# Performance work log

Measured on AMD Instinct MI355X. Metric: run time of the kernel, lower is better.

The kernel has to match this reference:

```python
import jax, jax.numpy as jnp
import numpy as np

HEADS = 4
DIM_HEAD = 64
EPS = 1e-12  # F.normalize clamp_min eps

def _l2norm(t):
    n = jnp.sqrt(jnp.sum(t * t, axis=-1, keepdims=True))
    return t / jnp.maximum(n, EPS)

def _dwconv3d(x, w, groups):
    # x: [b, c, d, h, w]; w: [c, 1, 3, 3, 3]
    return jax.lax.conv_general_dilated(
        x, w, window_strides=(1, 1, 1),
        padding=((1, 1), (1, 1), (1, 1)),
        dimension_numbers=('NCDHW', 'OIDHW', 'NCDHW'),
        feature_group_count=groups)

def setup_inputs() -> dict:
    key = jax.random.key(0)
    ks = jax.random.split(key, 6)
    dim, inner = 64, HEADS * DIM_HEAD
    x_in = jax.random.normal(ks[0], (1, 8, 128, 128, dim), jnp.float32)
    w_qkv = jax.random.normal(ks[1], (dim, 3 * inner), jnp.float32) * 0.05
    rescale = jnp.ones((HEADS, 1, 1), jnp.float32)
    w_proj = jax.random.normal(ks[2], (inner, dim), jnp.float32) * 0.05
    b_proj = jax.random.normal(ks[3], (dim,), jnp.float32) * 0.01
    w_pe1 = jax.random.normal(ks[4], (dim, 1, 3, 3, 3), jnp.float32) * 0.1
    w_pe2 = jax.random.normal(ks[5], (dim, 1, 3, 3, 3), jnp.float32) * 0.1
    return {"x_in": x_in, "w_qkv": w_qkv, "rescale": rescale,
            "w_proj": w_proj, "b_proj": b_proj, "w_pe1": w_pe1, "w_pe2": w_pe2}

def reference(x_in, w_qkv, rescale, w_proj, b_proj, w_pe1, w_pe2):
    b, d, h, w, c = x_in.shape
    N = d * h * w
    inner = HEADS * DIM_HEAD
    x = x_in.reshape(b, N, c)
    qkv = x @ w_qkv  # [b, N, 3*inner]
    q, k, v = jnp.split(qkv, 3, axis=-1)
    # [b, N, inner] -> [b, heads, dim_head, N]
    to_hdn = lambda t: t.reshape(b, N, HEADS, DIM_HEAD).transpose(0, 2, 3, 1)
    q, k, v = to_hdn(q), to_hdn(k), to_hdn(v)
    q = _l2norm(q)
    k = _l2norm(k)
    attn = jnp.einsum('bhdn,bhen->bhde', k, q)  # [b, heads, dd, dd]
    attn = attn * rescale[None]
    attn = jax.nn.softmax(attn, axis=-1)
    xo = jnp.einsum('bhde,bhen->bhdn', attn, v)  # [b, heads, dd, N]
    xo = xo.transpose(0, 3, 1, 2).reshape(b, N, inner)  # (h dd) channel order
    out_c = (xo @ w_proj + b_proj).reshape(b, d, h, w, c)
    # positional branch: depthwise conv3d -> GELU -> depthwise conv3d
    xp = x_in.transpose(0, 4, 1, 2, 3)  # [b, c, d, h, w]
    xp = _dwconv3d(xp, w_pe1, c)
    xp = jax.nn.gelu(xp, approximate=False)
    xp = _dwconv3d(xp, w_pe2, c)
    out_p = xp.transpose(0, 2, 3, 4, 1)
    return out_c + out_p
```

## Files before the change

kernel.cpp:

```cpp
#include <hip/hip_runtime.h>
#include <hip/hip_bf16.h>
#include <math.h>


#define NTOK 131072

typedef __attribute__((ext_vector_type(8))) short short8v;
typedef __attribute__((ext_vector_type(4))) float f32x4;

__device__ __forceinline__ uint32_t pk2(float a, float b) {
    return ((__float_as_uint(a) + 0x8000u) >> 16) |
           (((__float_as_uint(b) + 0x8000u) >> 16) << 16);
}
__device__ __forceinline__ float bl(uint32_t w) { return __uint_as_float(w << 16); }
__device__ __forceinline__ float bh(uint32_t w) { return __uint_as_float(w & 0xFFFF0000u); }

__global__ __launch_bounds__(256) void k_gram(const float* __restrict__ x,
                                              float* __restrict__ partial) {
    const int tid = threadIdx.x;
    const int lane = tid & 63;
    const int wave = tid >> 6;
    const int gwave = blockIdx.x * 4 + wave;
    const int lh = lane >> 4;
    const int lc = lane & 15;
    f32x4 acc[10];
#pragma unroll
    for (int t = 0; t < 10; ++t) acc[t] = (f32x4){0.f, 0.f, 0.f, 0.f};
    const long tokBase = (long)gwave * 64;
#pragma unroll
    for (int s = 0; s < 2; ++s) {
        const long t0 = tokBase + s * 32 + lh * 8;
        float v[4][8];
#pragma unroll
        for (int r = 0; r < 4; ++r) {
            const float* p = x + t0 * 64 + r * 16 + lc;
#pragma unroll
            for (int i = 0; i < 8; ++i) v[r][i] = p[i * 64];
        }
        union { short8v s8; uint32_t u[4]; } fh[4], fl[4];
#pragma unroll
        for (int r = 0; r < 4; ++r) {
#pragma unroll
            for (int w = 0; w < 4; ++w) {
                const float a = v[r][2 * w], b = v[r][2 * w + 1];
                const uint32_t hw = pk2(a, b);
                fh[r].u[w] = hw;
                fl[r].u[w] = pk2(a - bl(hw), b - bh(hw));
            }
        }
#pragma unroll
        for (int td = 0; td < 4; ++td) {
#pragma unroll
            for (int te = td; te < 4; ++te) {
                const int t = td * 4 + te - (td * (td + 1)) / 2;
                acc[t] = __builtin_amdgcn_mfma_f32_16x16x32_bf16(fh[td].s8, fh[te].s8, acc[t], 0, 0, 0);
                acc[t] = __builtin_amdgcn_mfma_f32_16x16x32_bf16(fh[td].s8, fl[te].s8, acc[t], 0, 0, 0);
                acc[t] = __builtin_amdgcn_mfma_f32_16x16x32_bf16(fl[td].s8, fh[te].s8, acc[t], 0, 0, 0);
            }
        }
    }
    float* pb = partial + (size_t)gwave * 2560;
#pragma unroll
    for (int t = 0; t < 10; ++t)
#pragma unroll
        for (int j = 0; j < 4; ++j)
            pb[t * 256 + (lh * 4 + j) * 16 + lc] = acc[t][j];
}

__global__ __launch_bounds__(256) void k_reduceG(const float* __restrict__ partial,
                                                 float* __restrict__ G) {
    const int entry = (blockIdx.x & 15) * 256 + threadIdx.x;
    const int slice = blockIdx.x >> 4;
    const int d = entry >> 6, e = entry & 63;
    int td = d >> 4, te = e >> 4, r = d & 15, c = e & 15;
    if (td > te) { int t = td; td = te; te = t; t = r; r = c; c = t; }
    const int off = (td * 4 + te - (td * (td + 1)) / 2) * 256 + r * 16 + c;
    const float* p = partial + (size_t)slice * 64 * 2560 + off;
    float s = 0.f;
#pragma unroll 8
    for (int i = 0; i < 64; ++i) s += p[(size_t)i * 2560];
    atomicAdd(&G[entry], s);
}

__global__ __launch_bounds__(512) void k_attn(const float* __restrict__ G,
                                              const float* __restrict__ w_qkv,
                                              const float* __restrict__ rescale,
                                              const float* __restrict__ w_proj,
                                              float* __restrict__ wf) {
    __shared__ float smem[6 * 4096 + 64 * 65];
    float (*Gs)[64] = (float(*)[64])smem;
    float (*PT)[64] = (float(*)[64])smem;
    float (*Bq)[64] = (float(*)[64])(smem + 4096);
    float (*Bk)[64] = (float(*)[64])(smem + 8192);
    float (*Bp)[64] = (float(*)[64])(smem + 12288);
    float (*M1)[64] = (float(*)[64])(smem + 16384);
    float (*M2)[64] = (float(*)[64])(smem + 20480);
    float (*Sb)[65] = (float(*)[65])(smem + 24576);
    __shared__ float qin[64], kin[64];

    const int h = blockIdx.x;
    const int tid = threadIdx.x;
    const int lane = tid & 63;
    const int g = tid >> 6;
    const int p0 = g * 8;

    for (int idx = tid; idx < 4096; idx += 512) {
        const int a = idx >> 6, e = idx & 63;
        Gs[a][e] = G[idx];
        Bq[a][e] = w_qkv[a * 768 + h * 64 + e];
        Bk[a][e] = w_qkv[a * 768 + 256 + h * 64 + e];
        Bp[a][e] = w_proj[(h * 64 + a) * 64 + e];
    }
    __syncthreads();

    {
        float acc[8];
#pragma unroll
        for (int i = 0; i < 8; ++i) acc[i] = 0.f;
        for (int a = 0; a < 64; ++a) {
            const float r = Bq[a][lane];
            const float4 l0 = *(const float4*)&Gs[a][p0];
            const float4 l1 = *(const float4*)&Gs[a][p0 + 4];
            acc[0] += l0.x * r; acc[1] += l0.y * r; acc[2] += l0.z * r; acc[3] += l0.w * r;
            acc[4] += l1.x * r; acc[5] += l1.y * r; acc[6] += l1.z * r; acc[7] += l1.w * r;
        }
#pragma unroll
        for (int i = 0; i < 8; ++i) M1[p0 + i][lane] = acc[i];
    }
    {
        float acc[8];
#pragma unroll
        for (int i = 0; i < 8; ++i) acc[i] = 0.f;
        for (int a = 0; a < 64; ++a) {
            const float r = Bk[a][lane];
            const float4 l0 = *(const float4*)&Gs[a][p0];
            const float4 l1 = *(const float4*)&Gs[a][p0 + 4];
            acc[0] += l0.x * r; acc[1] += l0.y * r; acc[2] += l0.z * r; acc[3] += l0.w * r;
            acc[4] += l1.x * r; acc[5] += l1.y * r; acc[6] += l1.z * r; acc[7] += l1.w * r;
        }
#pragma unroll
        for (int i = 0; i < 8; ++i) M2[p0 + i][lane] = acc[i];
    }
    __syncthreads();

    if (tid < 64) {
        float s = 0.f;
        for (int a = 0; a < 64; ++a) s += Bq[a][tid] * M1[a][tid];
        qin[tid] = 1.f / fmaxf(sqrtf(s), 1e-12f);
    } else if (tid < 128) {
        const int d = tid - 64;
        float s = 0.f;
        for (int a = 0; a < 64; ++a) s += Bk[a][d] * M2[a][d];
        kin[d] = 1.f / fmaxf(sqrtf(s), 1e-12f);
    }
    __syncthreads();

    const float rs = rescale[h];
    {
        float acc[8];
#pragma unroll
        for (int i = 0; i < 8; ++i) acc[i] = 0.f;
        for (int a = 0; a < 64; ++a) {
            const float r = M1[a][lane];
            const float4 l0 = *(const float4*)&Bk[a][p0];
            const float4 l1 = *(const float4*)&Bk[a][p0 + 4];
            acc[0] += l0.x * r; acc[1] += l0.y * r; acc[2] += l0.z * r; acc[3] += l0.w * r;
            acc[4] += l1.x * r; acc[5] += l1.y * r; acc[6] += l1.z * r; acc[7] += l1.w * r;
        }
        const float qv = qin[lane] * rs;
#pragma unroll
        for (int i = 0; i < 8; ++i) Sb[p0 + i][lane] = acc[i] * (kin[p0 + i] * qv);
    }
    for (int idx = tid; idx < 4096; idx += 512) {
        const int a = idx >> 6, e = idx & 63;
        Bq[e][a] = w_qkv[a * 768 + 512 + h * 64 + e];
    }
    __syncthreads();

    if (tid < 64) {
        const int d = tid;
        float m = -1e30f;
        for (int e = 0; e < 64; ++e) m = fmaxf(m, Sb[d][e]);
        float s = 0.f;
        for (int e = 0; e < 64; ++e) {
            const float pv = expf(Sb[d][e] - m);
            s += pv;
            PT[e][d] = pv;
        }
        const float inv = 1.f / s;
        for (int e = 0; e < 64; ++e) PT[e][d] *= inv;
    }
    __syncthreads();

    {
        float acc[8];
#pragma unroll
        for (int i = 0; i < 8; ++i) acc[i] = 0.f;
        for (int e = 0; e < 64; ++e) {
            const float r = Bq[e][lane];
            const float4 l0 = *(const float4*)&PT[e][p0];
            const float4 l1 = *(const float4*)&PT[e][p0 + 4];
            acc[0] += l0.x * r; acc[1] += l0.y * r; acc[2] += l0.z * r; acc[3] += l0.w * r;
            acc[4] += l1.x * r; acc[5] += l1.y * r; acc[6] += l1.z * r; acc[7] += l1.w * r;
        }
        __syncthreads();
#pragma unroll
        for (int i = 0; i < 8; ++i) M2[p0 + i][lane] = acc[i];
    }
    __syncthreads();

    {
        float acc[8];
#pragma unroll
        for (int i = 0; i < 8; ++i) acc[i] = 0.f;
        for (int d = 0; d < 64; ++d) {
            const float r = Bp[d][lane];
            const float4 l0 = *(const float4*)&M2[d][p0];
            const float4 l1 = *(const float4*)&M2[d][p0 + 4];
            acc[0] += l0.x * r; acc[1] += l0.y * r; acc[2] += l0.z * r; acc[3] += l0.w * r;
            acc[4] += l1.x * r; acc[5] += l1.y * r; acc[6] += l1.z * r; acc[7] += l1.w * r;
        }
#pragma unroll
        for (int i = 0; i < 8; ++i) atomicAdd(&wf[(p0 + i) * 64 + lane], acc[i]);
    }
}

__global__ __launch_bounds__(256) void k_out(const float* __restrict__ x,
                                             const float* __restrict__ wf_g,
                                             const float* __restrict__ b_proj,
                                             float* __restrict__ out) {
    const int tid = threadIdx.x;
    const int lane = tid & 63;
    const int wave = tid >> 6;
    const int lr = lane & 15;
    const int kg = lane >> 4;

    union { short8v s8; uint32_t u[4]; } wfh[2][4], wfl[2][4];
#pragma unroll
    for (int ks = 0; ks < 2; ++ks)
#pragma unroll
        for (int nt = 0; nt < 4; ++nt)
#pragma unroll
            for (int w = 0; w < 4; ++w) {
                const int k0 = ks * 32 + kg * 8 + 2 * w;
                const float a = wf_g[k0 * 64 + nt * 16 + lr];
                const float b = wf_g[(k0 + 1) * 64 + nt * 16 + lr];
                const uint32_t hw = pk2(a, b);
                wfh[ks][nt].u[w] = hw;
                wfl[ks][nt].u[w] = pk2(a - bl(hw), b - bh(hw));
            }
    float bb[4];
#pragma unroll
    for (int nt = 0; nt < 4; ++nt) bb[nt] = b_proj[nt * 16 + lr];

    const long strip0 = ((long)blockIdx.x * 4 + wave) * 2;
#pragma unroll
    for (int s = 0; s < 2; ++s) {
        const long tok0 = (strip0 + s) * 16;
        union { short8v s8; uint32_t u[4]; } ah[2], al[2];
#pragma unroll
        for (int ks = 0; ks < 2; ++ks) {
            const float* p = x + (tok0 + lr) * 64 + ks * 32 + kg * 8;
            const float4 a0 = *(const float4*)p;
            const float4 a1 = *(const float4*)(p + 4);
            const float va[8] = {a0.x, a0.y, a0.z, a0.w, a1.x, a1.y, a1.z, a1.w};
#pragma unroll
            for (int w = 0; w < 4; ++w) {
                const uint32_t hw = pk2(va[2 * w], va[2 * w + 1]);
                ah[ks].u[w] = hw;
                al[ks].u[w] = pk2(va[2 * w] - bl(hw), va[2 * w + 1] - bh(hw));
            }
        }
        f32x4 acc[4];
#pragma unroll
        for (int nt = 0; nt < 4; ++nt) acc[nt] = (f32x4){0.f, 0.f, 0.f, 0.f};
#pragma unroll
        for (int ks = 0; ks < 2; ++ks)
#pragma unroll
            for (int nt = 0; nt < 4; ++nt) {
                acc[nt] = __builtin_amdgcn_mfma_f32_16x16x32_bf16(ah[ks].s8, wfh[ks][nt].s8, acc[nt], 0, 0, 0);
                acc[nt] = __builtin_amdgcn_mfma_f32_16x16x32_bf16(ah[ks].s8, wfl[ks][nt].s8, acc[nt], 0, 0, 0);
                acc[nt] = __builtin_amdgcn_mfma_f32_16x16x32_bf16(al[ks].s8, wfh[ks][nt].s8, acc[nt], 0, 0, 0);
            }
#pragma unroll
        for (int nt = 0; nt < 4; ++nt)
#pragma unroll
            for (int j = 0; j < 4; ++j)
                out[(tok0 + kg * 4 + j) * 64 + nt * 16 + lr] = acc[nt][j] + bb[nt];
    }
}

__global__ __launch_bounds__(256) void k_conv(const float* __restrict__ x,
                                              const float* __restrict__ w1,
                                              const float* __restrict__ w2,
                                              float* __restrict__ out) {
    __shared__ float xt[12][12][8][10];
    __shared__ uint32_t y1[10][10][8][5];
    const int tid = threadIdx.x;
    const int b = blockIdx.x;
    const int xcd = b & 7, seq = (b >> 3) & 31, cg = b >> 8;
    const int tile = xcd * 32 + seq;
    const int tw = tile & 15, th = tile >> 4;
    const int h0 = th * 8, w0 = tw * 8;
    const int c = tid & 7;
    const int cglob = cg * 8 + c;

    float wr1[27];
#pragma unroll
    for (int o = 0; o < 27; ++o) wr1[o] = w1[cglob * 27 + o];

    for (int e = tid; e < 1152; e += 256) {
        const int sp = e >> 3;
        const int hh = sp / 12;
        const int ww = sp - hh * 12;
        const int gh = h0 + hh - 2, gw = w0 + ww - 2;
        float col[10];
#pragma unroll
        for (int i = 0; i < 10; ++i) col[i] = 0.f;
        if ((unsigned)gh < 128u && (unsigned)gw < 128u) {
            const float* xp = x + ((long)gh * 128 + gw) * 64 + cglob;
#pragma unroll
            for (int gd = 0; gd < 8; ++gd) col[gd + 1] = xp[(long)gd * 1048576];
        }
        float* dst = &xt[hh][ww][e & 7][0];
#pragma unroll
        for (int i = 0; i < 5; ++i) *(float2*)(dst + 2 * i) = make_float2(col[2 * i], col[2 * i + 1]);
    }
    __syncthreads();

    for (int e = tid; e < 800; e += 256) {
        const int sp = e >> 3;
        const int hi_ = sp / 10;
        const int wi = sp - hi_ * 10;
        const int ghp = h0 + hi_ - 1, gwp = w0 + wi - 1;
        uint32_t ow_[5];
        if ((unsigned)ghp < 128u && (unsigned)gwp < 128u) {
            float acc[8];
#pragma unroll
            for (int j = 0; j < 8; ++j) acc[j] = 0.f;
#pragma unroll
            for (int oh = 0; oh < 3; ++oh) {
#pragma unroll
                for (int ow = 0; ow < 3; ++ow) {
                    const float* cp = &xt[hi_ + oh][wi + ow][e & 7][0];
                    float xc[10];
#pragma unroll
                    for (int s2 = 0; s2 < 5; ++s2) {
                        const float2 t = *(const float2*)(cp + 2 * s2);
                        xc[2 * s2] = t.x; xc[2 * s2 + 1] = t.y;
                    }
                    const float wg0 = wr1[oh * 3 + ow];
                    const float wg1 = wr1[9 + oh * 3 + ow];
                    const float wg2 = wr1[18 + oh * 3 + ow];
#pragma unroll
                    for (int j = 0; j < 8; ++j)
                        acc[j] += wg0 * xc[j] + wg1 * xc[j + 1] + wg2 * xc[j + 2];
                }
            }
            float gl[8];
#pragma unroll
            for (int j = 0; j < 8; ++j)
                gl[j] = 0.5f * acc[j] * (1.f + erff(acc[j] * 0.70710678118654752f));
            ow_[0] = pk2(0.f, gl[0]);
            ow_[1] = pk2(gl[1], gl[2]);
            ow_[2] = pk2(gl[3], gl[4]);
            ow_[3] = pk2(gl[5], gl[6]);
            ow_[4] = pk2(gl[7], 0.f);
        } else {
#pragma unroll
            for (int i = 0; i < 5; ++i) ow_[i] = 0u;
        }
        uint32_t* dst = &y1[hi_][wi][e & 7][0];
#pragma unroll
        for (int i = 0; i < 5; ++i) dst[i] = ow_[i];
    }

    float wr2[27];
#pragma unroll
    for (int o = 0; o < 27; ++o) wr2[o] = w2[cglob * 27 + o];
    __syncthreads();

    for (int e = tid; e < 512; e += 256) {
        const int sp = e >> 3;
        const int ho = sp >> 3, wo = sp & 7;
        float a2[8];
#pragma unroll
        for (int j = 0; j < 8; ++j) a2[j] = 0.f;
#pragma unroll
        for (int oh = 0; oh < 3; ++oh) {
#pragma unroll
            for (int ow = 0; ow < 3; ++ow) {
                const uint32_t* cp = &y1[ho + oh][wo + ow][e & 7][0];
                float yc[10];
#pragma unroll
                for (int wdx = 0; wdx < 5; ++wdx) {
                    const uint32_t wv = cp[wdx];
                    yc[2 * wdx] = bl(wv);
                    yc[2 * wdx + 1] = bh(wv);
                }
                const float wg0 = wr2[oh * 3 + ow];
                const float wg1 = wr2[9 + oh * 3 + ow];
                const float wg2 = wr2[18 + oh * 3 + ow];
#pragma unroll
                for (int j = 0; j < 8; ++j)
                    a2[j] += wg0 * yc[j] + wg1 * yc[j + 1] + wg2 * yc[j + 2];
            }
        }
        const int gh = h0 + ho, gw = w0 + wo;
        float* op = out + ((long)gh * 128 + gw) * 64 + cglob;
#pragma unroll
        for (int j = 0; j < 8; ++j) op[(long)j * 1048576] += a2[j];
    }
}

extern "C" void kernel_launch(void* const* d_in, const int* in_sizes, int n_in,
                              void* d_out, int out_size, void* d_ws, size_t ws_size,
                              hipStream_t stream) {
    const float* x       = (const float*)d_in[0];
    const float* w_qkv   = (const float*)d_in[1];
    const float* rescale = (const float*)d_in[2];
    const float* w_proj  = (const float*)d_in[3];
    const float* b_proj  = (const float*)d_in[4];
    const float* w_pe1   = (const float*)d_in[5];
    const float* w_pe2   = (const float*)d_in[6];
    float* out = (float*)d_out;

    float* G  = (float*)d_ws;
    float* wf = G + 4096;
    float* partial = out;

    hipMemsetAsync(G, 0, 8192 * sizeof(float), stream);
    k_gram<<<512, 256, 0, stream>>>(x, partial);
    k_reduceG<<<512, 256, 0, stream>>>(partial, G);
    k_attn<<<4, 512, 0, stream>>>(G, w_qkv, rescale, w_proj, wf);
    k_out<<<1024, 256, 0, stream>>>(x, wf, b_proj, out);
    k_conv<<<2048, 256, 0, stream>>>(x, w_pe1, w_pe2, out);
}
```

Baseline: 207.2 us.

## Reduce gram partials in-block, write conv result as bf16 to workspace

k_gram now sums its four waves' partial Gram tiles in shared memory before writing one partial per block, which cuts partial-buffer traffic and lets k_reduceG run with fewer blocks. It also zeroes G and wf itself, so the separate memset launch is gone. The conv input load now reads float4 channel vectors in token-major order and stores bf16 in LDS, replacing strided scalar loads. When workspace allows, the conv branch writes bf16 results to a scratch buffer that k_out adds during its store, avoiding a float read-modify-write of out; this adds bf16 rounding of the conv output and of its input tile.

```diff
diff --git a/kernel.cpp b/kernel.cpp
--- a/kernel.cpp
+++ b/kernel.cpp
@@ -12,21 +12,28 @@
     return ((__float_as_uint(a) + 0x8000u) >> 16) |
            (((__float_as_uint(b) + 0x8000u) >> 16) << 16);
 }
+__device__ __forceinline__ uint16_t pk1(float a) {
+    return (uint16_t)((__float_as_uint(a) + 0x8000u) >> 16);
+}
 __device__ __forceinline__ float bl(uint32_t w) { return __uint_as_float(w << 16); }
 __device__ __forceinline__ float bh(uint32_t w) { return __uint_as_float(w & 0xFFFF0000u); }
 
 __global__ __launch_bounds__(256) void k_gram(const float* __restrict__ x,
-                                              float* __restrict__ partial) {
+                                              float* __restrict__ partial,
+                                              float* __restrict__ Gwf) {
+    __shared__ float lred[3][2560];
     const int tid = threadIdx.x;
     const int lane = tid & 63;
     const int wave = tid >> 6;
-    const int gwave = blockIdx.x * 4 + wave;
     const int lh = lane >> 4;
     const int lc = lane & 15;
+    if (blockIdx.x == 0) {
+        for (int i = tid; i < 8192; i += 256) Gwf[i] = 0.f;
+    }
     f32x4 acc[10];
 #pragma unroll
     for (int t = 0; t < 10; ++t) acc[t] = (f32x4){0.f, 0.f, 0.f, 0.f};
-    const long tokBase = (long)gwave * 64;
+    const long tokBase = ((long)blockIdx.x * 4 + wave) * 64;
 #pragma unroll
     for (int s = 0; s < 2; ++s) {
         const long t0 = tokBase + s * 32 + lh * 8;
@@ -59,12 +66,24 @@
             }
         }
     }
-    float* pb = partial + (size_t)gwave * 2560;
-#pragma unroll
-    for (int t = 0; t < 10; ++t)
-#pragma unroll
-        for (int j = 0; j < 4; ++j)
-            pb[t * 256 + (lh * 4 + j) * 16 + lc] = acc[t][j];
+    if (wave != 0) {
+#pragma unroll
+        for (int t = 0; t < 10; ++t)
+#pragma unroll
+            for (int j = 0; j < 4; ++j)
+                lred[wave - 1][t * 256 + (lh * 4 + j) * 16 + lc] = acc[t][j];
+    }
+    __syncthreads();
+    if (wave == 0) {
+        float* pb = partial + (size_t)blockIdx.x * 2560;
+#pragma unroll
+        for (int t = 0; t < 10; ++t)
+#pragma unroll
+            for (int j = 0; j < 4; ++j) {
+                const int e = t * 256 + (lh * 4 + j) * 16 + lc;
+                pb[e] = acc[t][j] + lred[0][e] + lred[1][e] + lred[2][e];
+            }
+    }
 }
 
 __global__ __launch_bounds__(256) void k_reduceG(const float* __restrict__ partial,
@@ -225,76 +244,13 @@
     }
 }
 
-__global__ __launch_bounds__(256) void k_out(const float* __restrict__ x,
-                                             const float* __restrict__ wf_g,
-                                             const float* __restrict__ b_proj,
-                                             float* __restrict__ out) {
-    const int tid = threadIdx.x;
-    const int lane = tid & 63;
-    const int wave = tid >> 6;
-    const int lr = lane & 15;
-    const int kg = lane >> 4;
-
-    union { short8v s8; uint32_t u[4]; } wfh[2][4], wfl[2][4];
-#pragma unroll
-    for (int ks = 0; ks < 2; ++ks)
-#pragma unroll
-        for (int nt = 0; nt < 4; ++nt)
-#pragma unroll
-            for (int w = 0; w < 4; ++w) {
-                const int k0 = ks * 32 + kg * 8 + 2 * w;
-                const float a = wf_g[k0 * 64 + nt * 16 + lr];
-                const float b = wf_g[(k0 + 1) * 64 + nt * 16 + lr];
-                const uint32_t hw = pk2(a, b);
-                wfh[ks][nt].u[w] = hw;
-                wfl[ks][nt].u[w] = pk2(a - bl(hw), b - bh(hw));
-            }
-    float bb[4];
-#pragma unroll
-    for (int nt = 0; nt < 4; ++nt) bb[nt] = b_proj[nt * 16 + lr];
-
-    const long strip0 = ((long)blockIdx.x * 4 + wave) * 2;
-#pragma unroll
-    for (int s = 0; s < 2; ++s) {
-        const long tok0 = (strip0 + s) * 16;
-        union { short8v s8; uint32_t u[4]; } ah[2], al[2];
-#pragma unroll
-        for (int ks = 0; ks < 2; ++ks) {
-            const float* p = x + (tok0 + lr) * 64 + ks * 32 + kg * 8;
-            const float4 a0 = *(const float4*)p;
-            const float4 a1 = *(const float4*)(p + 4);
-            const float va[8] = {a0.x, a0.y, a0.z, a0.w, a1.x, a1.y, a1.z, a1.w};
-#pragma unroll
-            for (int w = 0; w < 4; ++w) {
-                const uint32_t hw = pk2(va[2 * w], va[2 * w + 1]);
-                ah[ks].u[w] = hw;
-                al[ks].u[w] = pk2(va[2 * w] - bl(hw), va[2 * w + 1] - bh(hw));
-            }
-        }
-        f32x4 acc[4];
-#pragma unroll
-        for (int nt = 0; nt < 4; ++nt) acc[nt] = (f32x4){0.f, 0.f, 0.f, 0.f};
-#pragma unroll
-        for (int ks = 0; ks < 2; ++ks)
-#pragma unroll
-            for (int nt = 0; nt < 4; ++nt) {
-                acc[nt] = __builtin_amdgcn_mfma_f32_16x16x32_bf16(ah[ks].s8, wfh[ks][nt].s8, acc[nt], 0, 0, 0);
-                acc[nt] = __builtin_amdgcn_mfma_f32_16x16x32_bf16(ah[ks].s8, wfl[ks][nt].s8, acc[nt], 0, 0, 0);
-                acc[nt] = __builtin_amdgcn_mfma_f32_16x16x32_bf16(al[ks].s8, wfh[ks][nt].s8, acc[nt], 0, 0, 0);
-            }
-#pragma unroll
-        for (int nt = 0; nt < 4; ++nt)
-#pragma unroll
-            for (int j = 0; j < 4; ++j)
-                out[(tok0 + kg * 4 + j) * 64 + nt * 16 + lr] = acc[nt][j] + bb[nt];
-    }
-}
-
+template <int WS>
 __global__ __launch_bounds__(256) void k_conv(const float* __restrict__ x,
                                               const float* __restrict__ w1,
                                               const float* __restrict__ w2,
-                                              float* __restrict__ out) {
-    __shared__ float xt[12][12][8][10];
+                                              float* __restrict__ out,
+                                              uint16_t* __restrict__ cws) {
+    __shared__ uint32_t xt[12][12][5][8];
     __shared__ uint32_t y1[10][10][8][5];
     const int tid = threadIdx.x;
     const int b = blockIdx.x;
@@ -309,22 +265,36 @@
 #pragma unroll
     for (int o = 0; o < 27; ++o) wr1[o] = w1[cglob * 27 + o];
 
-    for (int e = tid; e < 1152; e += 256) {
-        const int sp = e >> 3;
+    for (int e = tid; e < 288; e += 256) {
+        const int cq = e & 1;
+        const int sp = e >> 1;
         const int hh = sp / 12;
         const int ww = sp - hh * 12;
         const int gh = h0 + hh - 2, gw = w0 + ww - 2;
-        float col[10];
-#pragma unroll
-        for (int i = 0; i < 10; ++i) col[i] = 0.f;
+        uint32_t wv[5][4];
+#pragma unroll
+        for (int s = 0; s < 5; ++s)
+#pragma unroll
+            for (int cc = 0; cc < 4; ++cc) wv[s][cc] = 0u;
         if ((unsigned)gh < 128u && (unsigned)gw < 128u) {
-            const float* xp = x + ((long)gh * 128 + gw) * 64 + cglob;
-#pragma unroll
-            for (int gd = 0; gd < 8; ++gd) col[gd + 1] = xp[(long)gd * 1048576];
-        }
-        float* dst = &xt[hh][ww][e & 7][0];
-#pragma unroll
-        for (int i = 0; i < 5; ++i) *(float2*)(dst + 2 * i) = make_float2(col[2 * i], col[2 * i + 1]);
+            float a[8][4];
+#pragma unroll
+            for (int gd = 0; gd < 8; ++gd) {
+                const float4 q = *(const float4*)(x + (((long)gd * 16384 + gh * 128 + gw)) * 64 + cg * 8 + cq * 4);
+                a[gd][0] = q.x; a[gd][1] = q.y; a[gd][2] = q.z; a[gd][3] = q.w;
+            }
+#pragma unroll
+            for (int cc = 0; cc < 4; ++cc) {
+                wv[0][cc] = pk2(0.f, a[0][cc]);
+                wv[1][cc] = pk2(a[1][cc], a[2][cc]);
+                wv[2][cc] = pk2(a[3][cc], a[4][cc]);
+                wv[3][cc] = pk2(a[5][cc], a[6][cc]);
+                wv[4][cc] = pk2(a[7][cc], 0.f);
+            }
+        }
+#pragma unroll
+        for (int s = 0; s < 5; ++s)
+            *(uint4*)&xt[hh][ww][s][cq * 4] = make_uint4(wv[s][0], wv[s][1], wv[s][2], wv[s][3]);
     }
     __syncthreads();
 
@@ -342,19 +312,20 @@
             for (int oh = 0; oh < 3; ++oh) {
 #pragma unroll
                 for (int ow = 0; ow < 3; ++ow) {
-                    const float* cp = &xt[hi_ + oh][wi + ow][e & 7][0];
-                    float xc[10];
-#pragma unroll
-                    for (int s2 = 0; s2 < 5; ++s2) {
-                        const float2 t = *(const float2*)(cp + 2 * s2);
-                        xc[2 * s2] = t.x; xc[2 * s2 + 1] = t.y;
+                    const uint32_t* cp = &xt[hi_ + oh][wi + ow][0][e & 7];
+                    float xc[11];
+#pragma unroll
+                    for (int wdx = 0; wdx < 5; ++wdx) {
+                        const uint32_t wv = cp[wdx * 8];
+                        xc[2 * wdx + 1] = bl(wv);
+                        xc[2 * wdx + 2] = bh(wv);
                     }
                     const float wg0 = wr1[oh * 3 + ow];
                     const float wg1 = wr1[9 + oh * 3 + ow];
                     const float wg2 = wr1[18 + oh * 3 + ow];
 #pragma unroll
                     for (int j = 0; j < 8; ++j)
-                        acc[j] += wg0 * xc[j] + wg1 * xc[j + 1] + wg2 * xc[j + 2];
+                        acc[j] += wg0 * xc[j + 1] + wg1 * xc[j + 2] + wg2 * xc[j + 3];
                 }
             }
             float gl[8];
@@ -407,9 +378,86 @@
             }
         }
         const int gh = h0 + ho, gw = w0 + wo;
-        float* op = out + ((long)gh * 128 + gw) * 64 + cglob;
-#pragma unroll
-        for (int j = 0; j < 8; ++j) op[(long)j * 1048576] += a2[j];
+        if (WS) {
+#pragma unroll
+            for (int j = 0; j < 8; ++j)
+                cws[(((long)j * 16384 + gh * 128 + gw)) * 64 + cglob] = pk1(a2[j]);
+        } else {
+            float* op = out + ((long)gh * 128 + gw) * 64 + cglob;
+#pragma unroll
+            for (int j = 0; j < 8; ++j) op[(long)j * 1048576] += a2[j];
+        }
+    }
+}
+
+template <int WS>
+__global__ __launch_bounds__(256) void k_out(const float* __restrict__ x,
+                                             const float* __restrict__ wf_g,
+                                             const float* __restrict__ b_proj,
+                                             const uint16_t* __restrict__ cws,
+                                             float* __restrict__ out) {
+    const int tid = threadIdx.x;
+    const int lane = tid & 63;
+    const int wave = tid >> 6;
+    const int lr = lane & 15;
+    const int kg = lane >> 4;
+
+    union { short8v s8; uint32_t u[4]; } wfh[2][4], wfl[2][4];
+#pragma unroll
+    for (int ks = 0; ks < 2; ++ks)
+#pragma unroll
+        for (int nt = 0; nt < 4; ++nt)
+#pragma unroll
+            for (int w = 0; w < 4; ++w) {
+                const int k0 = ks * 32 + kg * 8 + 2 * w;
+                const float a = wf_g[k0 * 64 + nt * 16 + lr];
+                const float b = wf_g[(k0 + 1) * 64 + nt * 16 + lr];
+                const uint32_t hw = pk2(a, b);
+                wfh[ks][nt].u[w] = hw;
+                wfl[ks][nt].u[w] = pk2(a - bl(hw), b - bh(hw));
+            }
+    float bb[4];
+#pragma unroll
+    for (int nt = 0; nt < 4; ++nt) bb[nt] = b_proj[nt * 16 + lr];
+
+    const long strip0 = ((long)blockIdx.x * 4 + wave) * 2;
+#pragma unroll
+    for (int s = 0; s < 2; ++s) {
+        const long tok0 = (strip0 + s) * 16;
+        union { short8v s8; uint32_t u[4]; } ah[2], al[2];
+#pragma unroll
+        for (int ks = 0; ks < 2; ++ks) {
+            const float* p = x + (tok0 + lr) * 64 + ks * 32 + kg * 8;
+            const float4 a0 = *(const float4*)p;
+            const float4 a1 = *(const float4*)(p + 4);
+            const float va[8] = {a0.x, a0.y, a0.z, a0.w, a1.x, a1.y, a1.z, a1.w};
+#pragma unroll
+            for (int w = 0; w < 4; ++w) {
+                const uint32_t hw = pk2(va[2 * w], va[2 * w + 1]);
+                ah[ks].u[w] = hw;
+                al[ks].u[w] = pk2(va[2 * w] - bl(hw), va[2 * w + 1] - bh(hw));
+            }
+        }
+        f32x4 acc[4];
+#pragma unroll
+        for (int nt = 0; nt < 4; ++nt) acc[nt] = (f32x4){0.f, 0.f, 0.f, 0.f};
+#pragma unroll
+        for (int ks = 0; ks < 2; ++ks)
+#pragma unroll
+            for (int nt = 0; nt < 4; ++nt) {
+                acc[nt] = __builtin_amdgcn_mfma_f32_16x16x32_bf16(ah[ks].s8, wfh[ks][nt].s8, acc[nt], 0, 0, 0);
+                acc[nt] = __builtin_amdgcn_mfma_f32_16x16x32_bf16(ah[ks].s8, wfl[ks][nt].s8, acc[nt], 0, 0, 0);
+                acc[nt] = __builtin_amdgcn_mfma_f32_16x16x32_bf16(al[ks].s8, wfh[ks][nt].s8, acc[nt], 0, 0, 0);
+            }
+#pragma unroll
+        for (int nt = 0; nt < 4; ++nt)
+#pragma unroll
+            for (int j = 0; j < 4; ++j) {
+                const long idx = (tok0 + kg * 4 + j) * 64 + nt * 16 + lr;
+                float v = acc[nt][j] + bb[nt];
+                if (WS) v += __uint_as_float(((uint32_t)cws[idx]) << 16);
+                out[idx] = v;
+            }
     }
 }
 
@@ -425,14 +473,22 @@
     const float* w_pe2   = (const float*)d_in[6];
     float* out = (float*)d_out;
 
-    float* G  = (float*)d_ws;
+    char* wsb = (char*)d_ws;
+    float* G  = (float*)wsb;
     float* wf = G + 4096;
+    uint16_t* cws = (uint16_t*)(wsb + 32768);
     float* partial = out;
 
-    hipMemsetAsync(G, 0, 8192 * sizeof(float), stream);
-    k_gram<<<512, 256, 0, stream>>>(x, partial);
-    k_reduceG<<<512, 256, 0, stream>>>(partial, G);
+    const bool ws_ok = ws_size >= (size_t)32768 + (size_t)NTOK * 64 * 2;
+
+    k_gram<<<512, 256, 0, stream>>>(x, partial, G);
+    k_reduceG<<<128, 256, 0, stream>>>(partial, G);
     k_attn<<<4, 512, 0, stream>>>(G, w_qkv, rescale, w_proj, wf);
-    k_out<<<1024, 256, 0, stream>>>(x, wf, b_proj, out);
-    k_conv<<<2048, 256, 0, stream>>>(x, w_pe1, w_pe2, out);
-}
+    if (ws_ok) {
+        k_conv<1><<<2048, 256, 0, stream>>>(x, w_pe1, w_pe2, nullptr, cws);
+        k_out<1><<<1024, 256, 0, stream>>>(x, wf, b_proj, cws, out);
+    } else {
+        k_out<0><<<1024, 256, 0, stream>>>(x, wf, b_proj, nullptr, out);
+        k_conv<0><<<2048, 256, 0, stream>>>(x, w_pe1, w_pe2, out, nullptr);
+    }
+}
```

After: 188.4 us. 1.1x faster.
